# Kernel optimization log

Measured on AMD Instinct MI355X. Metric: run time of the kernel, lower is better.

The kernel has to match this reference:

```python
import jax, jax.numpy as jnp
import numpy as np

FPFM = 256.0
B = 2097152
C = 32


def _integerize(v, scale):
    # Mirrors ArmInt.set_param_from_float: round-half-away-from-zero to int,
    # stored back as float (pure_int=False path).
    fv = v * scale
    fv = fv + jnp.sign(fv) * 0.5
    return jnp.trunc(fv)  # trunc toward zero == torch .to(int32)


def setup_inputs() -> dict:
    key = jax.random.key(0)
    ks = jax.random.split(key, 8)
    x = jax.random.normal(ks[0], (B, C), dtype=jnp.float32)
    # float-domain params (small, residual-friendly), then integerized
    w0 = _integerize(jax.random.normal(ks[1], (C, C), jnp.float32) * 0.05, FPFM)
    b0 = _integerize(jax.random.normal(ks[2], (C,), jnp.float32) * 0.05, FPFM * FPFM)
    w1 = _integerize(jax.random.normal(ks[3], (C, C), jnp.float32) * 0.05, FPFM)
    b1 = _integerize(jax.random.normal(ks[4], (C,), jnp.float32) * 0.05, FPFM * FPFM)
    w_out = _integerize(jax.random.normal(ks[5], (2, C), jnp.float32) * 0.05, FPFM)
    b_out = _integerize(jax.random.normal(ks[6], (2,), jnp.float32) * 0.05, FPFM * FPFM)
    return {"x": x, "w0": w0, "b0": b0, "w1": w1, "b1": b1,
            "w_out": w_out, "b_out": b_out}


def _arm_layer(h, W, b, residual):
    # F.linear + optional residual scaled by FPFM
    xx = h @ W.T + b
    if residual:
        xx = xx + h * FPFM
    # emulated integer rounding: add sign*FPFM/2, divide, trunc toward zero
    xx = xx + jnp.sign(xx) * (FPFM / 2.0)
    # where(xx<0, -(-xx/f), xx/f) is identity in float; trunc matches .to(int32)
    return jnp.trunc(xx / FPFM)


def reference(x, w0, b0, w1, b1, w_out, b_out):
    h = x * FPFM  # fixed-point lift (pure_int=False: stays float)
    h = jax.nn.relu(_arm_layer(h, w0, b0, True))
    h = jax.nn.relu(_arm_layer(h, w1, b1, True))
    h = _arm_layer(h, w_out, b_out, False)
    raw = h / FPFM  # [B, 2]
    mu = raw[:, 0]
    log_scale = raw[:, 1]
    scale = jnp.exp(jnp.clip(log_scale - 4.0, -4.6, 5.0))
    return mu, scale, log_scale
```

## Files before the change

kernel.cpp:

```cpp
#include <hip/hip_runtime.h>
#include <math.h>


typedef __attribute__((ext_vector_type(8))) short bf16x8;
typedef __attribute__((ext_vector_type(4))) float f32x4;

#define MFMA16(A, B, C) __builtin_amdgcn_mfma_f32_16x16x32_bf16((A), (B), (C), 0, 0, 0)

__device__ inline short bf_top(float v) {
    return (short)(__float_as_uint(v) >> 16);
}
__device__ inline float bf_topf(float v) {
    return __uint_as_float(__float_as_uint(v) & 0xffff0000u);
}

__global__ __launch_bounds__(256)
void armint_mfma(const float* __restrict__ x,
                 const float* __restrict__ w0, const float* __restrict__ b0,
                 const float* __restrict__ w1, const float* __restrict__ b1,
                 const float* __restrict__ wo, const float* __restrict__ bo,
                 float* __restrict__ out, int nrows)
{
    __shared__ float lds_all[4][32 * 36];

    const int lane = threadIdx.x & 63;
    const int wave = threadIdx.x >> 6;
    const int lm   = lane & 15;
    const int quad = lane >> 4;
    float* lds = lds_all[wave];

    const size_t nn = (size_t)nrows;
    const size_t rowbase = (size_t)blockIdx.x * 128 + (size_t)wave * 32;

    bf16x8 w0f[2], w1f[2], wof;
    float b0v[2], b1v[2], bov;
    #pragma unroll
    for (int hh = 0; hh < 2; ++hh) {
        const int n = lm + 16 * hh;
        const float* p0 = w0 + n * 32 + quad * 8;
        const float* p1 = w1 + n * 32 + quad * 8;
        #pragma unroll
        for (int j = 0; j < 8; ++j) {
            w0f[hh][j] = bf_top(p0[j]);
            w1f[hh][j] = bf_top(p1[j]);
        }
        b0v[hh] = b0[n] + 128.0f;
        b1v[hh] = b1[n] + 128.0f;
    }
    #pragma unroll
    for (int j = 0; j < 8; ++j)
        wof[j] = (lm < 2) ? bf_top(wo[lm * 32 + quad * 8 + j]) : (short)0;
    bov = (lm < 2) ? bo[lm] : 0.0f;

    bf16x8 a0[2], a1[2], a2[2];
    #pragma unroll
    for (int t = 0; t < 2; ++t) {
        const float* xp = x + (rowbase + (size_t)(t * 16 + lm)) * 32 + quad * 8;
        float4 v0 = *(const float4*)xp;
        float4 v1 = *(const float4*)(xp + 4);
        float h[8] = {v0.x, v0.y, v0.z, v0.w, v1.x, v1.y, v1.z, v1.w};
        #pragma unroll
        for (int j = 0; j < 8; ++j) h[j] *= 256.0f;

        const int base = (t * 16 + lm) * 36 + quad * 8;
        *(float4*)&lds[base]     = make_float4(h[0], h[1], h[2], h[3]);
        *(float4*)&lds[base + 4] = make_float4(h[4], h[5], h[6], h[7]);

        #pragma unroll
        for (int j = 0; j < 8; ++j) {
            float c0 = bf_topf(h[j]);
            a0[t][j] = bf_top(h[j]);
            float r1 = h[j] - c0;
            float c1 = bf_topf(r1);
            a1[t][j] = bf_top(r1);
            float r2 = r1 - c1;
            a2[t][j] = bf_top(r2);
        }
    }

    f32x4 acc[2][2];
    #pragma unroll
    for (int t = 0; t < 2; ++t)
        #pragma unroll
        for (int hh = 0; hh < 2; ++hh) {
            f32x4 c = {b0v[hh], b0v[hh], b0v[hh], b0v[hh]};
            c = MFMA16(a0[t], w0f[hh], c);
            c = MFMA16(a1[t], w0f[hh], c);
            c = MFMA16(a2[t], w0f[hh], c);
            acc[t][hh] = c;
        }
    #pragma unroll
    for (int t = 0; t < 2; ++t)
        #pragma unroll
        for (int hh = 0; hh < 2; ++hh)
            #pragma unroll
            for (int k = 0; k < 4; ++k) {
                const int idx = (t * 16 + quad * 4 + k) * 36 + lm + 16 * hh;
                float hres = lds[idx];
                float xx = fmaf(hres, 256.0f, acc[t][hh][k]);
                lds[idx] = fmaxf(truncf(xx * (1.0f / 256.0f)), 0.0f);
            }

    bf16x8 c0f[2], c1f[2];
    #pragma unroll
    for (int t = 0; t < 2; ++t) {
        const int base = (t * 16 + lm) * 36 + quad * 8;
        float4 v0 = *(float4*)&lds[base];
        float4 v1 = *(float4*)&lds[base + 4];
        float h[8] = {v0.x, v0.y, v0.z, v0.w, v1.x, v1.y, v1.z, v1.w};
        #pragma unroll
        for (int j = 0; j < 8; ++j) {
            float c0 = bf_topf(h[j]);
            c0f[t][j] = bf_top(h[j]);
            c1f[t][j] = bf_top(h[j] - c0);
        }
    }
    #pragma unroll
    for (int t = 0; t < 2; ++t)
        #pragma unroll
        for (int hh = 0; hh < 2; ++hh) {
            f32x4 c = {b1v[hh], b1v[hh], b1v[hh], b1v[hh]};
            c = MFMA16(c0f[t], w1f[hh], c);
            c = MFMA16(c1f[t], w1f[hh], c);
            acc[t][hh] = c;
        }
    #pragma unroll
    for (int t = 0; t < 2; ++t)
        #pragma unroll
        for (int hh = 0; hh < 2; ++hh)
            #pragma unroll
            for (int k = 0; k < 4; ++k) {
                const int idx = (t * 16 + quad * 4 + k) * 36 + lm + 16 * hh;
                float hres = lds[idx];
                float xx = fmaf(hres, 256.0f, acc[t][hh][k]);
                lds[idx] = fmaxf(truncf(xx * (1.0f / 256.0f)), 0.0f);
            }

    bf16x8 d0f[2], d1f[2];
    #pragma unroll
    for (int t = 0; t < 2; ++t) {
        const int base = (t * 16 + lm) * 36 + quad * 8;
        float4 v0 = *(float4*)&lds[base];
        float4 v1 = *(float4*)&lds[base + 4];
        float h[8] = {v0.x, v0.y, v0.z, v0.w, v1.x, v1.y, v1.z, v1.w};
        #pragma unroll
        for (int j = 0; j < 8; ++j) {
            float c0 = bf_topf(h[j]);
            d0f[t][j] = bf_top(h[j]);
            d1f[t][j] = bf_top(h[j] - c0);
        }
    }
    #pragma unroll
    for (int t = 0; t < 2; ++t) {
        f32x4 c = {bov, bov, bov, bov};
        c = MFMA16(d0f[t], wof, c);
        c = MFMA16(d1f[t], wof, c);

        float o[4];
        #pragma unroll
        for (int k = 0; k < 4; ++k) {
            float a = c[k];
            float adj = a + copysignf(128.0f, a);
            o[k] = truncf(adj * (1.0f / 256.0f)) * (1.0f / 256.0f);
        }
        const size_t row = rowbase + (size_t)(t * 16 + quad * 4);
        if (lm == 0) {
            *(float4*)(out + row) = make_float4(o[0], o[1], o[2], o[3]);
        }
        if (lm == 1) {
            *(float4*)(out + 2 * nn + row) = make_float4(o[0], o[1], o[2], o[3]);
            float s[4];
            #pragma unroll
            for (int k = 0; k < 4; ++k)
                s[k] = expf(fminf(fmaxf(o[k] - 4.0f, -4.6f), 5.0f));
            *(float4*)(out + nn + row) = make_float4(s[0], s[1], s[2], s[3]);
        }
    }
}

extern "C" void kernel_launch(void* const* d_in, const int* in_sizes, int n_in,
                              void* d_out, int out_size, void* d_ws, size_t ws_size,
                              hipStream_t stream) {
    const float* x  = (const float*)d_in[0];
    const float* w0 = (const float*)d_in[1];
    const float* b0 = (const float*)d_in[2];
    const float* w1 = (const float*)d_in[3];
    const float* b1 = (const float*)d_in[4];
    const float* wo = (const float*)d_in[5];
    const float* bo = (const float*)d_in[6];
    float* out = (float*)d_out;

    int nrows = in_sizes[0] / 32;
    int grid = nrows / 128;

    armint_mfma<<<grid, 256, 0, stream>>>(x, w0, b0, w1, b1, wo, bo, out, nrows);
}
```

Measured before the change: 418.4 us.

## Fold residual and scaling into preprocessed split-bf16 weights via prep kernel

Adds a one-block prep kernel that folds the residual identity (256 on the diagonal) and the 1/256 scales into the weights and biases. It splits each weight into hi/lo bf16 parts and stores them in the workspace. The main kernel loads these ready-made fragments instead of converting fp32 weights, skips storing the input to LDS, and drops the residual read-modify-write epilogue. In exchange it issues more MFMAs per layer (hi/lo weight terms) and adds a second kernel launch, and the scaled weights carry rounding risk at the truncation boundaries.

```diff
diff --git a/kernel.cpp b/kernel.cpp
--- a/kernel.cpp
+++ b/kernel.cpp
@@ -14,12 +14,40 @@
     return __uint_as_float(__float_as_uint(v) & 0xffff0000u);
 }
 
+
+__global__ void armint_prep(const float* __restrict__ w0, const float* __restrict__ b0,
+                            const float* __restrict__ w1, const float* __restrict__ b1,
+                            const float* __restrict__ wo, const float* __restrict__ bo,
+                            short* __restrict__ ws, float* __restrict__ bsf)
+{
+    int t = threadIdx.x;
+    for (int i = t; i < 1024; i += 256) {
+        int n = i >> 5, k = i & 31;
+        float diag = (n == k) ? 256.0f : 0.0f;
+
+        float a = w0[i] + diag;
+        float ahi = bf_topf(a);
+        ws[i]          = bf_top(a);
+        ws[1024 + i]   = bf_top(a - ahi);
+
+        float b = (w1[i] + diag) * (1.0f / 256.0f);
+        float bhi = bf_topf(b);
+        ws[2048 + i]   = bf_top(b);
+        ws[3072 + i]   = bf_top(b - bhi);
+
+        float c = (n < 2) ? wo[n * 32 + k] * (1.0f / 256.0f) : 0.0f;
+        ws[4096 + i]   = bf_top(c);
+    }
+    if (t < 32) {
+        bsf[t]      = (b0[t] + 128.0f) * (1.0f / 256.0f);
+        bsf[32 + t] = (b1[t] + 128.0f) * (1.0f / 256.0f);
+        bsf[64 + t] = (t < 2) ? bo[t] * (1.0f / 256.0f) : 0.0f;
+    }
+}
+
 __global__ __launch_bounds__(256)
-void armint_mfma(const float* __restrict__ x,
-                 const float* __restrict__ w0, const float* __restrict__ b0,
-                 const float* __restrict__ w1, const float* __restrict__ b1,
-                 const float* __restrict__ wo, const float* __restrict__ bo,
-                 float* __restrict__ out, int nrows)
+void armint_mfma(const float* __restrict__ x, const short* __restrict__ ws,
+                 const float* __restrict__ bias, float* __restrict__ out, int nrows)
 {
     __shared__ float lds_all[4][32 * 36];
 
@@ -32,25 +60,21 @@
     const size_t nn = (size_t)nrows;
     const size_t rowbase = (size_t)blockIdx.x * 128 + (size_t)wave * 32;
 
-    bf16x8 w0f[2], w1f[2], wof;
-    float b0v[2], b1v[2], bov;
+    bf16x8 w0hi[2], w0lo[2], w1hi[2], w1lo[2], wof;
+    float bs0[2], bs1[2];
     #pragma unroll
     for (int hh = 0; hh < 2; ++hh) {
         const int n = lm + 16 * hh;
-        const float* p0 = w0 + n * 32 + quad * 8;
-        const float* p1 = w1 + n * 32 + quad * 8;
-        #pragma unroll
-        for (int j = 0; j < 8; ++j) {
-            w0f[hh][j] = bf_top(p0[j]);
-            w1f[hh][j] = bf_top(p1[j]);
-        }
-        b0v[hh] = b0[n] + 128.0f;
-        b1v[hh] = b1[n] + 128.0f;
-    }
-    #pragma unroll
-    for (int j = 0; j < 8; ++j)
-        wof[j] = (lm < 2) ? bf_top(wo[lm * 32 + quad * 8 + j]) : (short)0;
-    bov = (lm < 2) ? bo[lm] : 0.0f;
+        const int o = n * 32 + quad * 8;
+        w0hi[hh] = *(const bf16x8*)(ws + o);
+        w0lo[hh] = *(const bf16x8*)(ws + 1024 + o);
+        w1hi[hh] = *(const bf16x8*)(ws + 2048 + o);
+        w1lo[hh] = *(const bf16x8*)(ws + 3072 + o);
+        bs0[hh] = bias[n];
+        bs1[hh] = bias[32 + n];
+    }
+    wof = *(const bf16x8*)(ws + 4096 + lm * 32 + quad * 8);
+    const float bsov = bias[64 + lm];
 
     bf16x8 a0[2], a1[2], a2[2];
     #pragma unroll
@@ -59,13 +83,6 @@
         float4 v0 = *(const float4*)xp;
         float4 v1 = *(const float4*)(xp + 4);
         float h[8] = {v0.x, v0.y, v0.z, v0.w, v1.x, v1.y, v1.z, v1.w};
-        #pragma unroll
-        for (int j = 0; j < 8; ++j) h[j] *= 256.0f;
-
-        const int base = (t * 16 + lm) * 36 + quad * 8;
-        *(float4*)&lds[base]     = make_float4(h[0], h[1], h[2], h[3]);
-        *(float4*)&lds[base + 4] = make_float4(h[4], h[5], h[6], h[7]);
-
         #pragma unroll
         for (int j = 0; j < 8; ++j) {
             float c0 = bf_topf(h[j]);
@@ -73,8 +90,7 @@
             float r1 = h[j] - c0;
             float c1 = bf_topf(r1);
             a1[t][j] = bf_top(r1);
-            float r2 = r1 - c1;
-            a2[t][j] = bf_top(r2);
+            a2[t][j] = bf_top(r1 - c1);
         }
     }
 
@@ -83,10 +99,12 @@
     for (int t = 0; t < 2; ++t)
         #pragma unroll
         for (int hh = 0; hh < 2; ++hh) {
-            f32x4 c = {b0v[hh], b0v[hh], b0v[hh], b0v[hh]};
-            c = MFMA16(a0[t], w0f[hh], c);
-            c = MFMA16(a1[t], w0f[hh], c);
-            c = MFMA16(a2[t], w0f[hh], c);
+            f32x4 c = {bs0[hh], bs0[hh], bs0[hh], bs0[hh]};
+            c = MFMA16(a0[t], w0hi[hh], c);
+            c = MFMA16(a1[t], w0hi[hh], c);
+            c = MFMA16(a2[t], w0hi[hh], c);
+            c = MFMA16(a0[t], w0lo[hh], c);
+            c = MFMA16(a1[t], w0lo[hh], c);
             acc[t][hh] = c;
         }
     #pragma unroll
@@ -94,12 +112,9 @@
         #pragma unroll
         for (int hh = 0; hh < 2; ++hh)
             #pragma unroll
-            for (int k = 0; k < 4; ++k) {
-                const int idx = (t * 16 + quad * 4 + k) * 36 + lm + 16 * hh;
-                float hres = lds[idx];
-                float xx = fmaf(hres, 256.0f, acc[t][hh][k]);
-                lds[idx] = fmaxf(truncf(xx * (1.0f / 256.0f)), 0.0f);
-            }
+            for (int k = 0; k < 4; ++k)
+                lds[(t * 16 + quad * 4 + k) * 36 + lm + 16 * hh] =
+                    fmaxf(truncf(acc[t][hh][k]), 0.0f);
 
     bf16x8 c0f[2], c1f[2];
     #pragma unroll
@@ -119,9 +134,11 @@
     for (int t = 0; t < 2; ++t)
         #pragma unroll
         for (int hh = 0; hh < 2; ++hh) {
-            f32x4 c = {b1v[hh], b1v[hh], b1v[hh], b1v[hh]};
-            c = MFMA16(c0f[t], w1f[hh], c);
-            c = MFMA16(c1f[t], w1f[hh], c);
+            f32x4 c = {bs1[hh], bs1[hh], bs1[hh], bs1[hh]};
+            c = MFMA16(c0f[t], w1hi[hh], c);
+            c = MFMA16(c1f[t], w1hi[hh], c);
+            c = MFMA16(c0f[t], w1lo[hh], c);
+            c = MFMA16(c1f[t], w1lo[hh], c);
             acc[t][hh] = c;
         }
     #pragma unroll
@@ -129,12 +146,9 @@
         #pragma unroll
         for (int hh = 0; hh < 2; ++hh)
             #pragma unroll
-            for (int k = 0; k < 4; ++k) {
-                const int idx = (t * 16 + quad * 4 + k) * 36 + lm + 16 * hh;
-                float hres = lds[idx];
-                float xx = fmaf(hres, 256.0f, acc[t][hh][k]);
-                lds[idx] = fmaxf(truncf(xx * (1.0f / 256.0f)), 0.0f);
-            }
+            for (int k = 0; k < 4; ++k)
+                lds[(t * 16 + quad * 4 + k) * 36 + lm + 16 * hh] =
+                    fmaxf(truncf(acc[t][hh][k]), 0.0f);
 
     bf16x8 d0f[2], d1f[2];
     #pragma unroll
@@ -152,7 +166,7 @@
     }
     #pragma unroll
     for (int t = 0; t < 2; ++t) {
-        f32x4 c = {bov, bov, bov, bov};
+        f32x4 c = {bsov, bsov, bsov, bsov};
         c = MFMA16(d0f[t], wof, c);
         c = MFMA16(d1f[t], wof, c);
 
@@ -160,8 +174,7 @@
         #pragma unroll
         for (int k = 0; k < 4; ++k) {
             float a = c[k];
-            float adj = a + copysignf(128.0f, a);
-            o[k] = truncf(adj * (1.0f / 256.0f)) * (1.0f / 256.0f);
+            o[k] = truncf(a + copysignf(0.5f, a)) * (1.0f / 256.0f);
         }
         const size_t row = rowbase + (size_t)(t * 16 + quad * 4);
         if (lm == 0) {
@@ -190,8 +203,12 @@
     const float* bo = (const float*)d_in[6];
     float* out = (float*)d_out;
 
+    short* ws  = (short*)d_ws;
+    float* bsf = (float*)((char*)d_ws + 10240);
+
     int nrows = in_sizes[0] / 32;
     int grid = nrows / 128;
 
-    armint_mfma<<<grid, 256, 0, stream>>>(x, w0, b0, w1, b1, wo, bo, out, nrows);
-}
+    armint_prep<<<1, 256, 0, stream>>>(w0, b0, w1, b1, wo, bo, ws, bsf);
+    armint_mfma<<<grid, 256, 0, stream>>>(x, ws, bsf, out, nrows);
+}
```

New measurement: 372.3 us. -11.0%, faster.
